# Optimization experiments

Measured on AMD Instinct MI355X. Metric: run time of the kernel, lower is better.

## Reference

```python
import jax, jax.numpy as jnp
import numpy as np


def _rbf_kernel(X, Z, variance, lengthscale):
    # K[n, r] = variance * exp(-||x_n - z_r||^2 / (2 * lengthscale^2))
    x2 = jnp.sum(X * X, axis=-1)[:, None]          # [N, 1]
    z2 = jnp.sum(Z * Z, axis=-1)[None, :]          # [1, R]
    sq = x2 + z2 - 2.0 * (X @ Z.T)                 # [N, R]
    sq = jnp.maximum(sq, 0.0)
    return variance * jnp.exp(-0.5 * sq / (lengthscale * lengthscale))


def setup_inputs() -> dict:
    key = jax.random.key(0)
    ks = jax.random.split(key, 6)
    N, D, S, F, R = 16384, 8, 8, 1024, 2048
    X_star = jax.random.normal(ks[0], (N, D), dtype=jnp.float32)
    ref_points = jax.random.normal(ks[1], (R, D), dtype=jnp.float32)
    omega = jax.random.normal(ks[2], (S, D, F), dtype=jnp.float32)
    two_pi = 2.0 * np.pi
    phase = jax.random.uniform(ks[3], (S, F), dtype=jnp.float32) * two_pi
    feature_weights = jax.random.normal(ks[4], (S, F), dtype=jnp.float32)
    correction_weights = jax.random.normal(ks[5], (S, R), dtype=jnp.float32)
    variance = jnp.ones((), dtype=jnp.float32)
    lengthscale = jnp.ones((), dtype=jnp.float32)
    return {
        "X_star": X_star,
        "ref_points": ref_points,
        "omega": omega,
        "phase": phase,
        "feature_weights": feature_weights,
        "correction_weights": correction_weights,
        "variance": variance,
        "lengthscale": lengthscale,
    }


def reference(X_star, ref_points, omega, phase, feature_weights,
              correction_weights, variance, lengthscale):
    F = omega.shape[-1]
    # RFF prior paths: angles [S, N, F]
    angles = jnp.einsum('nd,sdf->snf', X_star, omega) / lengthscale + phase[:, None, :]
    scale = jnp.sqrt(2.0 * variance / F)
    features = scale * jnp.cos(angles)                       # [S, N, F]
    prior = jnp.sum(features * feature_weights[:, None, :], axis=-1)  # [S, N]
    # Kernel correction term
    K_cross = _rbf_kernel(X_star, ref_points, variance, lengthscale)  # [N, R]
    update = jnp.einsum('nr,sr->sn', K_cross, correction_weights)     # [S, N]
    # mean_fn is None -> zero mean
    mean = jnp.zeros(X_star.shape[0], dtype=X_star.dtype)
    return prior + update + mean[None, :]
```

## Files before the change

### kernel.cpp

```cpp
#include <hip/hip_runtime.h>
#include <math.h>

#ifndef __has_builtin
#define __has_builtin(x) 0
#endif

typedef __attribute__((ext_vector_type(8))) short bf16x8;
typedef __attribute__((ext_vector_type(4))) float f32x4;

__device__ __forceinline__ float fast_fract(float x) {
#if __has_builtin(__builtin_amdgcn_fractf)
    return __builtin_amdgcn_fractf(x);
#else
    return x - floorf(x);
#endif
}
__device__ __forceinline__ float fast_cos2pi(float x) {
#if __has_builtin(__builtin_amdgcn_cosf)
    return __builtin_amdgcn_cosf(x);
#else
    return cosf(x * 6.28318530717958647692f);
#endif
}
__device__ __forceinline__ float fast_exp2(float x) {
#if __has_builtin(__builtin_amdgcn_exp2f)
    return __builtin_amdgcn_exp2f(x);
#else
    return exp2f(x);
#endif
}
__device__ __forceinline__ unsigned short f2bf(float f) {
    unsigned u = __float_as_uint(f);
    return (unsigned short)((u + 0x7FFFu + ((u >> 16) & 1u)) >> 16);
}
__device__ __forceinline__ float bf2f(unsigned short b) {
    return __uint_as_float(((unsigned)b) << 16);
}
__device__ __forceinline__ unsigned packbf(float lo, float hi) {
    return (unsigned)f2bf(lo) | ((unsigned)f2bf(hi) << 16);
}

constexpr int kN = 16384, kD = 8, kS = 8, kF = 1024, kR = 2048;
constexpr float kInv2Pi = 0.15915494309189535f;
constexpr float kLog2e  = 1.4426950408889634f;
constexpr int kWsPrior = 512, kWsZ = 128, kWsCw = 64;
constexpr int kWsTiles = kWsPrior + kWsZ + kWsCw;
constexpr size_t kWsNeed = (size_t)kWsTiles * 64 * 16;

__global__ __launch_bounds__(256)
void prep_kernel(const float* __restrict__ omega, const float* __restrict__ phase,
                 const float* __restrict__ Z, const float* __restrict__ cw,
                 const float* __restrict__ lsp, uint4* __restrict__ ws,
                 float* __restrict__ out)
{
    if (blockIdx.x >= 176) {
        const int zid = (blockIdx.x - 176) * 256 + threadIdx.x;
        float4* o4 = reinterpret_cast<float4*>(out);
        #pragma unroll
        for (int j = 0; j < 4; ++j)
            o4[zid * 4 + j] = (float4){0.f, 0.f, 0.f, 0.f};
        return;
    }
    const int job  = blockIdx.x * 256 + threadIdx.x;
    const int lane = job & 63;
    const int tile = job >> 6;
    const int g = lane >> 4, c = lane & 15;

    const float inv_ls = 1.0f / lsp[0];
    const float m_ang  = kInv2Pi * inv_ls;
    const float L      = kLog2e * inv_ls * inv_ls;

    unsigned short h[8];
    if (tile < kWsPrior) {
        const int s = tile >> 6, ft = tile & 63, f = ft * 16 + c;
        const float* om = omega + s * (kD * kF);
        const float* ph = phase + s * kF;
        #pragma unroll
        for (int j = 0; j < 8; ++j) {
            const int k = g * 8 + j;
            unsigned short v = 0;
            if (k < 16) {
                v = f2bf(om[(k & 7) * kF + f] * m_ang);
            } else if (k < 24) {
                const float w = om[(k - 16) * kF + f] * m_ang;
                v = f2bf(w - bf2f(f2bf(w)));
            } else if (k == 24) {
                v = f2bf(ph[f] * kInv2Pi);
            } else if (k == 25) {
                const float p = ph[f] * kInv2Pi;
                v = f2bf(p - bf2f(f2bf(p)));
            }
            h[j] = v;
        }
    } else if (tile < kWsPrior + kWsZ) {
        const int rt = tile - kWsPrior;
        const int r  = rt * 16 + c;
        const float* zr = Z + r * kD;
        float zz = 0.f;
        #pragma unroll
        for (int d = 0; d < kD; ++d) zz = fmaf(zr[d], zr[d], zz);
        const float ztv = -0.5f * L * zz;
        #pragma unroll
        for (int j = 0; j < 8; ++j) {
            const int k = g * 8 + j;
            unsigned short v = 0;
            if (k < 8) {
                v = f2bf(L * zr[k]);
            } else if (k < 16) {
                v = f2bf(L * zr[k - 8]);
            } else if (k < 24) {
                const float w = L * zr[k - 16];
                v = f2bf(w - bf2f(f2bf(w)));
            } else if (k == 24) {
                v = f2bf(ztv);
            } else if (k == 25) {
                v = f2bf(ztv - bf2f(f2bf(ztv)));
            } else if (k < 28) {
                v = 0x3F80;
            }
            h[j] = v;
        }
    } else {
        const int rb = tile - kWsPrior - kWsZ;
        const int r0 = rb * 32;
        #pragma unroll
        for (int j = 0; j < 8; ++j)
            h[j] = (c < 8) ? f2bf(cw[c * kR + r0 + g * 8 + j]) : (unsigned short)0;
    }
    uint4 w;
    w.x = (unsigned)h[0] | ((unsigned)h[1] << 16);
    w.y = (unsigned)h[2] | ((unsigned)h[3] << 16);
    w.z = (unsigned)h[4] | ((unsigned)h[5] << 16);
    w.w = (unsigned)h[6] | ((unsigned)h[7] << 16);
    ws[tile * 64 + lane] = w;
}

__device__ __forceinline__ bf16x8 build_af_x(const float* __restrict__ X,
                                             int row, int g)
{
    float xv[kD];
    const float4 x0 = *reinterpret_cast<const float4*>(X + row * kD);
    const float4 x1 = *reinterpret_cast<const float4*>(X + row * kD + 4);
    xv[0]=x0.x; xv[1]=x0.y; xv[2]=x0.z; xv[3]=x0.w;
    xv[4]=x1.x; xv[5]=x1.y; xv[6]=x1.z; xv[7]=x1.w;
    bf16x8 af;
    if (g == 1) {
        #pragma unroll
        for (int j = 0; j < 8; ++j)
            af[j] = (short)f2bf(xv[j] - bf2f(f2bf(xv[j])));
    } else {
        #pragma unroll
        for (int j = 0; j < 8; ++j) af[j] = (short)f2bf(xv[j]);
    }
    return af;
}

__global__ __launch_bounds__(256, 6)
void fused_main(const float* __restrict__ X, const float* __restrict__ fw,
                const float* __restrict__ varp, const float* __restrict__ lsp,
                const uint4* __restrict__ wsP, const uint4* __restrict__ wsZ,
                const uint4* __restrict__ wsC, float* __restrict__ out)
{
    __shared__ unsigned b2raw[4][512];
    __shared__ f32x4 red[2][2][2][16];
    const int tid  = threadIdx.x;
    const int lane = tid & 63;
    const int w    = __builtin_amdgcn_readfirstlane(tid >> 6);
    const int c = lane & 15, g = lane >> 4;
    const int bid = blockIdx.x;
    const int btype = bid % 3;

    if (btype != 2) {
        const int pb = (bid / 3) * 2 + btype;
        const int s  = pb & 7;
        const int ng = pb >> 3;
        const int n0 = ng * 128 + w * 32;

        bf16x8 af0, af1;
        if (g == 3) {
            #pragma unroll
            for (int j = 0; j < 8; ++j) { af0[j] = 0; af1[j] = 0; }
            af0[0] = (short)0x3F80; af0[1] = (short)0x3F80;
            af1[0] = (short)0x3F80; af1[1] = (short)0x3F80;
        } else {
            af0 = build_af_x(X, n0 + c, g);
            af1 = build_af_x(X, n0 + 16 + c, g);
        }

        const float scale = sqrtf(2.0f * varp[0] / (float)kF);
        const uint4* bp  = wsP + s * 4096 + lane;
        const float* fwp = fw + s * kF + c;

        float acc[2][4];
        #pragma unroll
        for (int t = 0; t < 2; ++t)
            #pragma unroll
            for (int r = 0; r < 4; ++r) acc[t][r] = 0.f;

        uint4 b0 = bp[0], b1 = bp[64];
        f32x4 pd00, pd01, pd10, pd11;
        {
            const bf16x8 v0 = __builtin_bit_cast(bf16x8, b0);
            const bf16x8 v1 = __builtin_bit_cast(bf16x8, b1);
            pd00 = __builtin_amdgcn_mfma_f32_16x16x32_bf16(af0, v0, (f32x4){0.f,0.f,0.f,0.f}, 0, 0, 0);
            pd01 = __builtin_amdgcn_mfma_f32_16x16x32_bf16(af1, v0, (f32x4){0.f,0.f,0.f,0.f}, 0, 0, 0);
            pd10 = __builtin_amdgcn_mfma_f32_16x16x32_bf16(af0, v1, (f32x4){0.f,0.f,0.f,0.f}, 0, 0, 0);
            pd11 = __builtin_amdgcn_mfma_f32_16x16x32_bf16(af1, v1, (f32x4){0.f,0.f,0.f,0.f}, 0, 0, 0);
        }
        float cf0 = fwp[0], cf1 = fwp[16];
        b0 = bp[128]; b1 = bp[192];

        for (int it = 1; it < 32; ++it) {
            const int nx = (it + 1 < 32) ? it + 1 : it;
            const uint4 p0 = bp[nx * 128];
            const uint4 p1 = bp[nx * 128 + 64];
            const float nf0 = fwp[it * 32];
            const float nf1 = fwp[it * 32 + 16];
            const bf16x8 v0 = __builtin_bit_cast(bf16x8, b0);
            const bf16x8 v1 = __builtin_bit_cast(bf16x8, b1);
            const f32x4 nd00 = __builtin_amdgcn_mfma_f32_16x16x32_bf16(af0, v0, (f32x4){0.f,0.f,0.f,0.f}, 0, 0, 0);
            const f32x4 nd01 = __builtin_amdgcn_mfma_f32_16x16x32_bf16(af1, v0, (f32x4){0.f,0.f,0.f,0.f}, 0, 0, 0);
            const f32x4 nd10 = __builtin_amdgcn_mfma_f32_16x16x32_bf16(af0, v1, (f32x4){0.f,0.f,0.f,0.f}, 0, 0, 0);
            const f32x4 nd11 = __builtin_amdgcn_mfma_f32_16x16x32_bf16(af1, v1, (f32x4){0.f,0.f,0.f,0.f}, 0, 0, 0);
            #pragma unroll
            for (int r = 0; r < 4; ++r) {
                acc[0][r] = fmaf(cf0, fast_cos2pi(fast_fract(pd00[r])), acc[0][r]);
                acc[1][r] = fmaf(cf0, fast_cos2pi(fast_fract(pd01[r])), acc[1][r]);
                acc[0][r] = fmaf(cf1, fast_cos2pi(fast_fract(pd10[r])), acc[0][r]);
                acc[1][r] = fmaf(cf1, fast_cos2pi(fast_fract(pd11[r])), acc[1][r]);
            }
            pd00 = nd00; pd01 = nd01; pd10 = nd10; pd11 = nd11;
            cf0 = nf0; cf1 = nf1;
            b0 = p0; b1 = p1;
        }
        #pragma unroll
        for (int r = 0; r < 4; ++r) {
            acc[0][r] = fmaf(cf0, fast_cos2pi(fast_fract(pd00[r])), acc[0][r]);
            acc[1][r] = fmaf(cf0, fast_cos2pi(fast_fract(pd01[r])), acc[1][r]);
            acc[0][r] = fmaf(cf1, fast_cos2pi(fast_fract(pd10[r])), acc[0][r]);
            acc[1][r] = fmaf(cf1, fast_cos2pi(fast_fract(pd11[r])), acc[1][r]);
        }

        #pragma unroll
        for (int m = 1; m <= 8; m <<= 1)
            #pragma unroll
            for (int t = 0; t < 2; ++t)
                #pragma unroll
                for (int r = 0; r < 4; ++r)
                    acc[t][r] += __shfl_xor(acc[t][r], m);

        if (c == 0) {
            #pragma unroll
            for (int t = 0; t < 2; ++t) {
                float* o = out + s * kN + n0 + t * 16 + g * 4;
                #pragma unroll
                for (int r = 0; r < 4; ++r) atomicAdd(o + r, scale * acc[t][r]);
            }
        }
    } else {
        const int ub   = bid / 3;
        const int tl   = w >> 1, half = w & 1;
        const int n0   = (ub * 2 + tl) * 16;

        const float inv_ls = 1.0f / lsp[0];
        const float L = kLog2e * inv_ls * inv_ls;

        bf16x8 bf1;
        {
            float xv[kD];
            const float4 x0 = *reinterpret_cast<const float4*>(X + (n0 + c) * kD);
            const float4 x1 = *reinterpret_cast<const float4*>(X + (n0 + c) * kD + 4);
            xv[0]=x0.x; xv[1]=x0.y; xv[2]=x0.z; xv[3]=x0.w;
            xv[4]=x1.x; xv[5]=x1.y; xv[6]=x1.z; xv[7]=x1.w;
            if (g == 3) {
                float xx = 0.f;
                #pragma unroll
                for (int d = 0; d < kD; ++d) xx = fmaf(xv[d], xv[d], xx);
                const float xt = -0.5f * L * xx;
                const unsigned short th = f2bf(xt);
                const unsigned short tlw = f2bf(xt - bf2f(th));
                #pragma unroll
                for (int j = 0; j < 8; ++j) bf1[j] = 0;
                bf1[0] = (short)0x3F80; bf1[1] = (short)0x3F80;
                bf1[2] = (short)th;     bf1[3] = (short)tlw;
            } else if (g == 1) {
                #pragma unroll
                for (int j = 0; j < 8; ++j)
                    bf1[j] = (short)f2bf(xv[j] - bf2f(f2bf(xv[j])));
            } else {
                #pragma unroll
                for (int j = 0; j < 8; ++j) bf1[j] = (short)f2bf(xv[j]);
            }
        }

        const int wbase = (g >> 1) * 64 + c * 4 + (g & 1) * 2;
        const int rbase = (g >> 1) * 128 + (g & 1) * 64 + c * 4;
        unsigned* bb = &b2raw[w][0];

        const uint4* zp = wsZ + lane;
        const uint4* cp = wsC + lane;
        const int rb0 = half * 32;

        f32x4 acc = {0.f, 0.f, 0.f, 0.f};
        uint4 za = zp[(rb0 * 2) * 64];
        uint4 zb = zp[(rb0 * 2 + 1) * 64];
        uint4 cf_cur = cp[rb0 * 64];
        uint4 cf_prev = cf_cur;

        {
            const uint4 zan = zp[((rb0 + 1) * 2) * 64];
            const uint4 zbn = zp[((rb0 + 1) * 2 + 1) * 64];
            const uint4 cfn = cp[(rb0 + 1) * 64];
            const f32x4 e0 = __builtin_amdgcn_mfma_f32_16x16x32_bf16(
                __builtin_bit_cast(bf16x8, za), bf1, (f32x4){0.f,0.f,0.f,0.f}, 0, 0, 0);
            const f32x4 e1 = __builtin_amdgcn_mfma_f32_16x16x32_bf16(
                __builtin_bit_cast(bf16x8, zb), bf1, (f32x4){0.f,0.f,0.f,0.f}, 0, 0, 0);
            float K0[4], K1[4];
            #pragma unroll
            for (int r = 0; r < 4; ++r) {
                K0[r] = fast_exp2(fminf(e0[r], 0.f));
                K1[r] = fast_exp2(fminf(e1[r], 0.f));
            }
            uint2 w0; w0.x = packbf(K0[0], K0[1]); w0.y = packbf(K0[2], K0[3]);
            uint2 w1; w1.x = packbf(K1[0], K1[1]); w1.y = packbf(K1[2], K1[3]);
            *reinterpret_cast<uint2*>(&bb[wbase])       = w0;
            *reinterpret_cast<uint2*>(&bb[wbase + 128]) = w1;
            asm volatile("" ::: "memory");
            cf_prev = cf_cur; cf_cur = cfn; za = zan; zb = zbn;
        }

        for (int i = 1; i < 32; ++i) {
            const int rb = rb0 + i;
            const int rbn = (i < 31) ? rb + 1 : rb;
            const uint4 zan = zp[(rbn * 2) * 64];
            const uint4 zbn = zp[(rbn * 2 + 1) * 64];
            const uint4 cfn = cp[rbn * 64];

            const uint4 kprev = *reinterpret_cast<const uint4*>(
                &bb[rbase + ((i - 1) & 1) * 256]);

            const f32x4 e0 = __builtin_amdgcn_mfma_f32_16x16x32_bf16(
                __builtin_bit_cast(bf16x8, za), bf1, (f32x4){0.f,0.f,0.f,0.f}, 0, 0, 0);
            const f32x4 e1 = __builtin_amdgcn_mfma_f32_16x16x32_bf16(
                __builtin_bit_cast(bf16x8, zb), bf1, (f32x4){0.f,0.f,0.f,0.f}, 0, 0, 0);

            float K0[4], K1[4];
            #pragma unroll
            for (int r = 0; r < 4; ++r) {
                K0[r] = fast_exp2(fminf(e0[r], 0.f));
                K1[r] = fast_exp2(fminf(e1[r], 0.f));
            }
            uint2 w0; w0.x = packbf(K0[0], K0[1]); w0.y = packbf(K0[2], K0[3]);
            uint2 w1; w1.x = packbf(K1[0], K1[1]); w1.y = packbf(K1[2], K1[3]);
            *reinterpret_cast<uint2*>(&bb[wbase + (i & 1) * 256])       = w0;
            *reinterpret_cast<uint2*>(&bb[wbase + 128 + (i & 1) * 256]) = w1;
            asm volatile("" ::: "memory");

            acc = __builtin_amdgcn_mfma_f32_16x16x32_bf16(
                __builtin_bit_cast(bf16x8, cf_prev), __builtin_bit_cast(bf16x8, kprev),
                acc, 0, 0, 0);

            cf_prev = cf_cur; cf_cur = cfn; za = zan; zb = zbn;
        }

        {
            const uint4 kprev = *reinterpret_cast<const uint4*>(
                &bb[rbase + (31 & 1) * 256]);
            acc = __builtin_amdgcn_mfma_f32_16x16x32_bf16(
                __builtin_bit_cast(bf16x8, cf_prev), __builtin_bit_cast(bf16x8, kprev),
                acc, 0, 0, 0);
        }

        if (g < 2) red[tl][half][g][c] = acc;
        __syncthreads();

        {
            const int tl2 = tid >> 7, s = (tid >> 4) & 7, n = tid & 15;
            const float sum = red[tl2][0][s >> 2][n][s & 3]
                            + red[tl2][1][s >> 2][n][s & 3];
            const int idx = s * kN + (ub * 2 + tl2) * 16 + n;
            atomicAdd(out + idx, varp[0] * sum);
        }
    }
}

__global__ __launch_bounds__(512, 8)
void prior_fb(const float* __restrict__ X, const float* __restrict__ omega,
              const float* __restrict__ phase, const float* __restrict__ fw,
              const float* __restrict__ varp, const float* __restrict__ lsp,
              float* __restrict__ out)
{
    const int tid  = threadIdx.x;
    const int nloc = tid & 63;
    const int wave = __builtin_amdgcn_readfirstlane(tid >> 6);
    const int s    = blockIdx.y;
    const int n    = blockIdx.x * 64 + nloc;
    const float variance = varp[0];
    const float inv_ls   = 1.0f / lsp[0];
    const float scale = sqrtf(2.0f * variance / (float)kF);
    float xa[kD];
    {
        const float4 x0 = *reinterpret_cast<const float4*>(X + n * kD);
        const float4 x1 = *reinterpret_cast<const float4*>(X + n * kD + 4);
        const float m = inv_ls * kInv2Pi;
        xa[0]=x0.x*m; xa[1]=x0.y*m; xa[2]=x0.z*m; xa[3]=x0.w*m;
        xa[4]=x1.x*m; xa[5]=x1.y*m; xa[6]=x1.z*m; xa[7]=x1.w*m;
    }
    const float* om  = omega + s * (kD * kF);
    const float* ph  = phase + s * kF;
    const float* fwp = fw    + s * kF;
    const int f0 = wave * 128;
    float acc0 = 0.f, acc1 = 0.f;
    for (int fb = f0; fb < f0 + 128; fb += 8) {
        float cv[8];
        #pragma unroll
        for (int j = 0; j < 8; ++j) {
            float t = ph[fb + j] * kInv2Pi;
            #pragma unroll
            for (int d = 0; d < kD; ++d) t = fmaf(xa[d], om[d * kF + fb + j], t);
            cv[j] = fast_cos2pi(fast_fract(t));
        }
        #pragma unroll
        for (int j = 0; j < 8; j += 2) {
            acc0 = fmaf(fwp[fb + j], cv[j], acc0);
            acc1 = fmaf(fwp[fb + j + 1], cv[j + 1], acc1);
        }
    }
    __shared__ float red[8][64];
    red[wave][nloc] = acc0 + acc1;
    __syncthreads();
    if (tid < 64) {
        float t = 0.f;
        #pragma unroll
        for (int k = 0; k < 8; ++k) t += red[k][tid];
        out[s * kN + blockIdx.x * 64 + tid] = scale * t;
    }
}

__global__ __launch_bounds__(1024, 8)
void update_fb(const float* __restrict__ X, const float* __restrict__ Z,
               const float* __restrict__ cw, const float* __restrict__ varp,
               const float* __restrict__ lsp, float* __restrict__ out)
{
    const int tid  = threadIdx.x;
    const int nloc = tid & 63;
    const int wave = __builtin_amdgcn_readfirstlane(tid >> 6);
    const int n    = blockIdx.x * 64 + nloc;
    const float variance = varp[0];
    const float inv_ls   = 1.0f / lsp[0];
    const float L = kLog2e * inv_ls * inv_ls;
    __shared__ float zt_lds[kR];
    __shared__ float red[16][64][kS + 1];
    float x[kD];
    {
        const float4 x0 = *reinterpret_cast<const float4*>(X + n * kD);
        const float4 x1 = *reinterpret_cast<const float4*>(X + n * kD + 4);
        x[0]=x0.x; x[1]=x0.y; x[2]=x0.z; x[3]=x0.w;
        x[4]=x1.x; x[5]=x1.y; x[6]=x1.z; x[7]=x1.w;
    }
    for (int r = tid; r < kR; r += 1024) {
        const float4 z0 = *reinterpret_cast<const float4*>(Z + r * kD);
        const float4 z1 = *reinterpret_cast<const float4*>(Z + r * kD + 4);
        float z2 = z0.x*z0.x + z0.y*z0.y + z0.z*z0.z + z0.w*z0.w
                 + z1.x*z1.x + z1.y*z1.y + z1.z*z1.z + z1.w*z1.w;
        zt_lds[r] = -0.5f * L * z2;
    }
    __syncthreads();
    float xb[kD]; float x2 = 0.f;
    #pragma unroll
    for (int d = 0; d < kD; ++d) { xb[d] = x[d] * L; x2 = fmaf(x[d], x[d], x2); }
    const float xt = -0.5f * L * x2;
    float accU[2][kS];
    #pragma unroll
    for (int j = 0; j < kS; ++j) { accU[0][j] = 0.f; accU[1][j] = 0.f; }
    const int r0 = wave * 128;
    #pragma unroll 4
    for (int rr = 0; rr < 128; ++rr) {
        const int r = r0 + rr;
        float e = xt + zt_lds[r];
        #pragma unroll
        for (int d = 0; d < kD; ++d) e = fmaf(xb[d], Z[r * kD + d], e);
        e = fminf(e, 0.f);
        const float K = fast_exp2(e);
        #pragma unroll
        for (int j = 0; j < kS; ++j)
            accU[rr & 1][j] = fmaf(K, cw[j * kR + r], accU[rr & 1][j]);
    }
    #pragma unroll
    for (int j = 0; j < kS; ++j) red[wave][nloc][j] = accU[0][j] + accU[1][j];
    __syncthreads();
    if (tid < 512) {
        const int n2 = tid & 63;
        const int jj = tid >> 6;
        float tot = 0.f;
        #pragma unroll
        for (int k = 0; k < 16; ++k) tot += red[k][n2][jj];
        const int idx = jj * kN + blockIdx.x * 64 + n2;
        out[idx] = fmaf(variance, tot, out[idx]);
    }
}

extern "C" void kernel_launch(void* const* d_in, const int* in_sizes, int n_in,
                              void* d_out, int out_size, void* d_ws, size_t ws_size,
                              hipStream_t stream) {
    const float* X  = (const float*)d_in[0];
    const float* Z  = (const float*)d_in[1];
    const float* om = (const float*)d_in[2];
    const float* ph = (const float*)d_in[3];
    const float* fw = (const float*)d_in[4];
    const float* cw = (const float*)d_in[5];
    const float* vp = (const float*)d_in[6];
    const float* lp = (const float*)d_in[7];
    float* out = (float*)d_out;

    if (ws_size >= kWsNeed) {
        uint4* wsP = (uint4*)d_ws;
        uint4* wsZ = wsP + (size_t)kWsPrior * 64;
        uint4* wsC = wsP + (size_t)(kWsPrior + kWsZ) * 64;
        hipLaunchKernelGGL(prep_kernel, dim3(208), dim3(256), 0, stream,
                           om, ph, Z, cw, lp, wsP, out);
        hipLaunchKernelGGL(fused_main, dim3(1536), dim3(256), 0, stream,
                           X, fw, vp, lp, wsP, wsZ, wsC, out);
    } else {
        hipLaunchKernelGGL(prior_fb, dim3(kN / 64, kS), dim3(512), 0, stream,
                           X, om, ph, fw, vp, lp, out);
        hipLaunchKernelGGL(update_fb, dim3(kN / 64), dim3(1024), 0, stream,
                           X, Z, cw, vp, lp, out);
    }
}
```

Before: 100.1 us.

## Move last quarter of prior feature work into the correction kernel

The prior kernel's feature loop now covers 24 of 32 feature chunks. The remaining 8 chunks are computed at the end of the RBF-correction kernel, which accumulates them into the output with atomics. This rebalances work between the two kernels to fill idle compute in the correction kernel. The cost is more atomics, extra X fragment rebuilds, and longer correction-kernel blocks.

```diff
diff --git a/kernel.cpp b/kernel.cpp
--- a/kernel.cpp
+++ b/kernel.cpp
@@ -210,8 +210,8 @@
         float cf0 = fwp[0], cf1 = fwp[16];
         b0 = bp[128]; b1 = bp[192];
 
-        for (int it = 1; it < 32; ++it) {
-            const int nx = (it + 1 < 32) ? it + 1 : it;
+        for (int it = 1; it < 24; ++it) {
+            const int nx = (it + 1 < 24) ? it + 1 : it;
             const uint4 p0 = bp[nx * 128];
             const uint4 p1 = bp[nx * 128 + 64];
             const float nf0 = fwp[it * 32];
@@ -380,6 +380,73 @@
                             + red[tl2][1][s >> 2][n][s & 3];
             const int idx = s * kN + (ub * 2 + tl2) * 16 + n;
             atomicAdd(out + idx, varp[0] * sum);
+        }
+
+        {
+            const int pu  = ub * 2 + (w >> 1);
+            const int s2  = pu & 7;
+            const int ng2 = pu >> 3;
+            const int nb  = ng2 * 128 + (w & 1) * 64;
+            const float scale = sqrtf(2.0f * varp[0] / (float)kF);
+            const uint4* bpp  = wsP + s2 * 4096 + lane;
+            const float* fwpp = fw + s2 * kF + c;
+
+            for (int pass = 0; pass < 2; ++pass) {
+                const int n0p = nb + pass * 32;
+                bf16x8 af0, af1;
+                if (g == 3) {
+                    #pragma unroll
+                    for (int j = 0; j < 8; ++j) { af0[j] = 0; af1[j] = 0; }
+                    af0[0] = (short)0x3F80; af0[1] = (short)0x3F80;
+                    af1[0] = (short)0x3F80; af1[1] = (short)0x3F80;
+                } else {
+                    af0 = build_af_x(X, n0p + c, g);
+                    af1 = build_af_x(X, n0p + 16 + c, g);
+                }
+                float pacc[2][4];
+                #pragma unroll
+                for (int t = 0; t < 2; ++t)
+                    #pragma unroll
+                    for (int r = 0; r < 4; ++r) pacc[t][r] = 0.f;
+
+                for (int fp = 24; fp < 32; ++fp) {
+                    const uint4 pb0 = bpp[fp * 128];
+                    const uint4 pb1 = bpp[fp * 128 + 64];
+                    const float fv0 = fwpp[fp * 32];
+                    const float fv1 = fwpp[fp * 32 + 16];
+                    const bf16x8 v0 = __builtin_bit_cast(bf16x8, pb0);
+                    const bf16x8 v1 = __builtin_bit_cast(bf16x8, pb1);
+                    const f32x4 d00 = __builtin_amdgcn_mfma_f32_16x16x32_bf16(af0, v0, (f32x4){0.f,0.f,0.f,0.f}, 0, 0, 0);
+                    const f32x4 d01 = __builtin_amdgcn_mfma_f32_16x16x32_bf16(af1, v0, (f32x4){0.f,0.f,0.f,0.f}, 0, 0, 0);
+                    const f32x4 d10 = __builtin_amdgcn_mfma_f32_16x16x32_bf16(af0, v1, (f32x4){0.f,0.f,0.f,0.f}, 0, 0, 0);
+                    const f32x4 d11 = __builtin_amdgcn_mfma_f32_16x16x32_bf16(af1, v1, (f32x4){0.f,0.f,0.f,0.f}, 0, 0, 0);
+                    #pragma unroll
+                    for (int r = 0; r < 4; ++r) {
+                        pacc[0][r] = fmaf(fv0, fast_cos2pi(fast_fract(d00[r])), pacc[0][r]);
+                        pacc[1][r] = fmaf(fv0, fast_cos2pi(fast_fract(d01[r])), pacc[1][r]);
+                        pacc[0][r] = fmaf(fv1, fast_cos2pi(fast_fract(d10[r])), pacc[0][r]);
+                        pacc[1][r] = fmaf(fv1, fast_cos2pi(fast_fract(d11[r])), pacc[1][r]);
+                    }
+                }
+
+                #pragma unroll
+                for (int m = 1; m <= 8; m <<= 1)
+                    #pragma unroll
+                    for (int t = 0; t < 2; ++t)
+                        #pragma unroll
+                        for (int r = 0; r < 4; ++r)
+                            pacc[t][r] += __shfl_xor(pacc[t][r], m);
+
+                if (c == 0) {
+                    #pragma unroll
+                    for (int t = 0; t < 2; ++t) {
+                        float* o = out + s2 * kN + n0p + t * 16 + g * 4;
+                        #pragma unroll
+                        for (int r = 0; r < 4; ++r)
+                            atomicAdd(o + r, scale * pacc[t][r]);
+                    }
+                }
+            }
         }
     }
 }
```

Result: slower. 105.5 us (+5.5%).
